# Kernel tuning notes

Measured on AMD Instinct MI355X. Metric: run time of the kernel, lower is better.

Reference implementation:

```python
import jax, jax.numpy as jnp
import numpy as np

THETA = 1.2
XI = 0.3


def setup_inputs() -> dict:
    key = jax.random.key(0)
    k1, k2 = jax.random.split(key)
    B, D = 8192, 512
    x = jax.random.normal(k1, (B, D), dtype=jnp.float32)
    y = jax.random.randint(k2, (B,), 0, 1000, dtype=jnp.int64)
    return {"x": x, "y": y}


def reference(x, y):
    B = x.shape[0]
    # per-sample L2 normalization: n_i = x_i / ||x_i||
    n = x / jnp.linalg.norm(x, axis=1, keepdims=True)  # [B, D]
    # pairwise squared distances ||n_i - n_j||^2 = |n_i|^2 + |n_j|^2 - 2 n_i.n_j
    sq = jnp.sum(n * n, axis=1)                        # [B]
    G = n @ n.T                                        # [B, B]
    dist2 = sq[:, None] + sq[None, :] - 2.0 * G        # [B, B]
    # indicator: +1 if same label else -1 (symmetric)
    ind = jnp.where(y[:, None] == y[None, :], 1.0, -1.0)
    # original loops i in [0,B), j in [i,B): upper triangle including diagonal
    idx = jnp.arange(B)
    mask = (idx[None, :] >= idx[:, None]).astype(x.dtype)
    hinge = jnp.maximum(THETA - dist2, 0.0)
    total = jnp.sum(mask * (XI + ind * hinge))
    m_scalar = 1.0 / (B * B - B)
    return m_scalar * total
```

## Files before the change

### kernel.cpp

```cpp
#include <hip/hip_runtime.h>
#include <cstdint>
#include <cstddef>

#define THETA 1.2f
#define XI 0.3f
#define BDIM 8192
#define DDIM 512
#define NROWP 32
#define NCOLP 64
#define NUNITS 1056
#define GRID 512
#define NPAIRS_UP (((double)BDIM * (double)(BDIM + 1)) * 0.5)

typedef float f32x4 __attribute__((ext_vector_type(4)));
typedef int i32x8 __attribute__((ext_vector_type(8)));


__global__ __launch_bounds__(256) void normalize_rows(
    const float* __restrict__ x, unsigned char* __restrict__ nf8,
    float* __restrict__ sq, unsigned int* __restrict__ counter)
{
    if (blockIdx.x == 0 && threadIdx.x == 0) { *counter = 0u; }
    int row = blockIdx.x * 4 + (threadIdx.x >> 6);
    int l = threadIdx.x & 63;
    const float4* xr = (const float4*)(x + (size_t)row * DDIM);
    float4 f0 = xr[l];
    float4 f1 = xr[l + 64];
    float s = f0.x*f0.x + f0.y*f0.y + f0.z*f0.z + f0.w*f0.w
            + f1.x*f1.x + f1.y*f1.y + f1.z*f1.z + f1.w*f1.w;
    #pragma unroll
    for (int m = 1; m < 64; m <<= 1) s += __shfl_xor(s, m);
    float rn = rsqrtf(s);
    int pk0 = __builtin_amdgcn_cvt_pk_fp8_f32(f0.x * rn, f0.y * rn, 0, false);
    pk0     = __builtin_amdgcn_cvt_pk_fp8_f32(f0.z * rn, f0.w * rn, pk0, true);
    int pk1 = __builtin_amdgcn_cvt_pk_fp8_f32(f1.x * rn, f1.y * rn, 0, false);
    pk1     = __builtin_amdgcn_cvt_pk_fp8_f32(f1.z * rn, f1.w * rn, pk1, true);
    size_t base = (size_t)(row >> 4) * 4 * 2048;
    int within = ((row & 15) + ((l >> 3) & 3) * 16) * 32 + (l & 7) * 4;
    int kc0 = l >> 5;
    int kc1 = (l >> 5) + 2;
    *(int*)(nf8 + base + (size_t)kc0 * 2048 + within) = pk0;
    *(int*)(nf8 + base + (size_t)kc1 * 2048 + within) = pk1;
    if (l == 0) sq[row] = s * rn * rn;
}

__device__ __forceinline__ void decode_unit(int u, int& ti, int& tj) {
    int t = (int)((65.0f - sqrtf(65.0f * 65.0f - 4.0f * (float)u)) * 0.5f);
    if (t > 31) t = 31;
    while (t < 31 && (t + 1) * (65 - (t + 1)) <= u) ++t;
    while (t > 0 && t * (65 - t) > u) --t;
    ti = t;
    tj = 2 * t + (u - t * (65 - t));
}

__global__ __launch_bounds__(512, 2) void gram_hinge(
    const unsigned char* __restrict__ nf8, const float* __restrict__ sq,
    const int* __restrict__ y, double* __restrict__ part,
    unsigned int* __restrict__ counter, float* __restrict__ out)
{
    __shared__ unsigned char As[2][32768];
    __shared__ float wpart[8];
    __shared__ double dpart[8];
    __shared__ int is_last;

    int tid = threadIdx.x;
    int w = tid >> 6, l = tid & 63;
    int wr = w >> 2, wc = w & 3;
    int lr = l & 15, q = l >> 4;

    auto stageA = [&](unsigned char* dAb, int pti, int pc) {
        #pragma unroll
        for (int i = 0; i < 4; ++i) {
            int t = w * 4 + i;
            int rf = t >> 1, half = t & 1;
            const unsigned char* src = nf8
                + ((size_t)((pti * 16 + rf) * 4 + pc)) * 2048 + half * 1024 + l * 16;
            __builtin_amdgcn_global_load_lds(
                (const __attribute__((address_space(1))) void*)src,
                (__attribute__((address_space(3))) void*)(dAb + t * 1024), 16, 0, 0);
        }
    };
    auto bload = [&](int ptj, int pc, i32x8* dst) {
        #pragma unroll
        for (int ni = 0; ni < 2; ++ni)
            dst[ni] = *(const i32x8*)(nf8
                + ((size_t)((ptj * 8 + wc * 2 + ni) * 4 + pc)) * 2048 + l * 32);
    };

    float acc0 = 0.f, acc1 = 0.f;

    int u = blockIdx.x;
    int ti, tj;
    decode_unit(u, ti, tj);

    i32x8 bfe[2], bfo[2];

    bload(tj, 0, bfe);
    stageA(As[0], ti, 0);

    while (u < NUNITS) {
        int u_next = u + GRID;
        bool have_next = (u_next < NUNITS);
        int ti_n = 0, tj_n = 0;
        if (have_next) decode_unit(u_next, ti_n, tj_n);

        f32x4 accv[8][2] = {};

        #pragma unroll 1
        for (int cc = 0; cc < 2; ++cc) {
            bload(tj, 2 * cc + 1, bfo);
            stageA(As[1], ti, 2 * cc + 1);
            asm volatile("s_waitcnt vmcnt(8)" ::: "memory");
            asm volatile("s_barrier" ::: "memory");
            __builtin_amdgcn_s_setprio(1);
            #pragma unroll
            for (int mi = 0; mi < 8; ++mi) {
                i32x8 af = *(const i32x8*)(As[0] + (wr * 8 + mi) * 2048 + l * 32);
                #pragma unroll
                for (int ni = 0; ni < 2; ++ni)
                    accv[mi][ni] = __builtin_amdgcn_mfma_scale_f32_16x16x128_f8f6f4(
                        af, bfe[ni], accv[mi][ni],
                        0, 0, 0, 0x7F7F7F7F, 0, 0x7F7F7F7F);
            }
            __builtin_amdgcn_s_setprio(0);
            asm volatile("s_barrier" ::: "memory");

            bool more = (cc == 0) || have_next;
            int nti = (cc == 0) ? ti : ti_n;
            int ntj = (cc == 0) ? tj : tj_n;
            int nc  = (cc == 0) ? 2 : 0;
            if (more) {
                bload(ntj, nc, bfe);
                stageA(As[0], nti, nc);
                asm volatile("s_waitcnt vmcnt(8)" ::: "memory");
            } else {
                asm volatile("s_waitcnt vmcnt(0)" ::: "memory");
            }
            asm volatile("s_barrier" ::: "memory");
            __builtin_amdgcn_s_setprio(1);
            #pragma unroll
            for (int mi = 0; mi < 8; ++mi) {
                i32x8 af = *(const i32x8*)(As[1] + (wr * 8 + mi) * 2048 + l * 32);
                #pragma unroll
                for (int ni = 0; ni < 2; ++ni)
                    accv[mi][ni] = __builtin_amdgcn_mfma_scale_f32_16x16x128_f8f6f4(
                        af, bfo[ni], accv[mi][ni],
                        0, 0, 0, 0x7F7F7F7F, 0, 0x7F7F7F7F);
            }
            __builtin_amdgcn_s_setprio(0);
            asm volatile("s_barrier" ::: "memory");
        }

        {
            int jb = tj * 128 + wc * 32 + lr;
            float sqj[2]; int yj[2];
            #pragma unroll
            for (int ni = 0; ni < 2; ++ni) {
                sqj[ni] = sq[jb + ni * 16];
                yj[ni]  = y[jb + ni * 16];
            }
            bool skip = (tj == 2 * ti) && (wr == 1);
            bool full = (tj > 2 * ti + 1) || ((tj == 2 * ti + 1) && (wr == 0));
            if (!skip) {
                if (full) {
                    #pragma unroll
                    for (int mi = 0; mi < 8; ++mi) {
                        #pragma unroll
                        for (int r = 0; r < 4; ++r) {
                            int ia = ti * 256 + wr * 128 + mi * 16 + q * 4 + r;
                            float ci = THETA - sq[ia];
                            int yi = y[ia];
                            float h0 = fmaxf(fmaf(2.f, accv[mi][0][r], ci - sqj[0]), 0.f);
                            acc0 += (yi == yj[0]) ? h0 : -h0;
                            float h1 = fmaxf(fmaf(2.f, accv[mi][1][r], ci - sqj[1]), 0.f);
                            acc1 += (yi == yj[1]) ? h1 : -h1;
                        }
                    }
                } else {
                    #pragma unroll
                    for (int mi = 0; mi < 8; ++mi) {
                        #pragma unroll
                        for (int r = 0; r < 4; ++r) {
                            int rl_ = mi * 16 + q * 4 + r;
                            int ia = ti * 256 + wr * 128 + rl_;
                            float ci = THETA - sq[ia];
                            int yi = y[ia];
                            #pragma unroll
                            for (int ni = 0; ni < 2; ++ni) {
                                float h = fmaxf(fmaf(2.f, accv[mi][ni][r], ci - sqj[ni]), 0.f);
                                float sh = (yi == yj[ni]) ? h : -h;
                                if (wc * 32 + ni * 16 + lr >= rl_) acc0 += sh;
                            }
                        }
                    }
                }
            }
        }

        u = u_next; ti = ti_n; tj = tj_n;
    }

    float local = acc0 + acc1;
    #pragma unroll
    for (int off = 32; off > 0; off >>= 1) local += __shfl_down(local, off);
    if (l == 0) wpart[w] = local;
    __syncthreads();
    if (tid == 0) {
        double ssum = 0.0;
        #pragma unroll
        for (int i = 0; i < 8; ++i) ssum += (double)wpart[i];
        __hip_atomic_store(&part[blockIdx.x], ssum, __ATOMIC_RELEASE, __HIP_MEMORY_SCOPE_AGENT);
        unsigned int ticket = __hip_atomic_fetch_add(
            counter, 1u, __ATOMIC_ACQ_REL, __HIP_MEMORY_SCOPE_AGENT);
        is_last = (ticket == GRID - 1) ? 1 : 0;
    }
    __syncthreads();
    if (is_last) {
        double s = 0.0;
        for (int i = tid; i < GRID; i += 512)
            s += __hip_atomic_load(&part[i], __ATOMIC_ACQUIRE, __HIP_MEMORY_SCOPE_AGENT);
        #pragma unroll
        for (int off = 32; off > 0; off >>= 1) s += __shfl_down(s, off);
        if (l == 0) dpart[w] = s;
        __syncthreads();
        if (tid == 0) {
            double t8 = 0.0;
            #pragma unroll
            for (int i = 0; i < 8; ++i) t8 += dpart[i];
            double total = t8 + (double)XI * NPAIRS_UP;
            const double m = 1.0 / ((double)BDIM * (double)BDIM - (double)BDIM);
            out[0] = (float)(total * m);
        }
    }
}

extern "C" void kernel_launch(void* const* d_in, const int* in_sizes, int n_in,
                              void* d_out, int out_size, void* d_ws, size_t ws_size,
                              hipStream_t stream) {
    const float* x = (const float*)d_in[0];
    const int* y = (const int*)d_in[1];
    float* out = (float*)d_out;

    unsigned char* nf8 = (unsigned char*)d_ws;
    char* p = (char*)d_ws + (size_t)BDIM * DDIM;
    float* sq = (float*)p;
    unsigned int* counter = (unsigned int*)(p + (size_t)BDIM * 4);
    double* part = (double*)(p + (size_t)BDIM * 4 + 64);

    normalize_rows<<<BDIM / 4, 256, 0, stream>>>(x, nf8, sq, counter);
    gram_hinge<<<GRID, 512, 0, stream>>>(nf8, sq, y, part, counter, out);
}
```

Before: 117.3 us.

## Use square 256x256 tiles with B staged in LDS instead of 256x128

Changes the work unit from 256x128 tiles to 256x256 tiles over the upper triangle, halving the number of units and the grid size. The B operand is now staged through LDS with async global-to-LDS loads alongside A, rather than each wave loading B fragments straight from global memory into registers. The intent is higher arithmetic intensity per byte loaded and less redundant global traffic for B. The cost is twice the LDS footprint, 32 accumulator vectors per wave with more register pressure, and a grid of only 256 blocks, which may underfill the device.

Result: faster. 107.0 us (-8.8%).

```diff
diff --git a/kernel.cpp b/kernel.cpp
--- a/kernel.cpp
+++ b/kernel.cpp
@@ -6,10 +6,9 @@
 #define XI 0.3f
 #define BDIM 8192
 #define DDIM 512
-#define NROWP 32
-#define NCOLP 64
-#define NUNITS 1056
-#define GRID 512
+#define NPANEL 32
+#define NUNITS 528
+#define GRID 256
 #define NPAIRS_UP (((double)BDIM * (double)(BDIM + 1)) * 0.5)
 
 typedef float f32x4 __attribute__((ext_vector_type(4)));
@@ -45,12 +44,13 @@
 }
 
 __device__ __forceinline__ void decode_unit(int u, int& ti, int& tj) {
-    int t = (int)((65.0f - sqrtf(65.0f * 65.0f - 4.0f * (float)u)) * 0.5f);
+    int t = (int)((65.0f - sqrtf(4225.0f - 8.0f * (float)u)) * 0.5f);
+    if (t < 0) t = 0;
     if (t > 31) t = 31;
-    while (t < 31 && (t + 1) * (65 - (t + 1)) <= u) ++t;
-    while (t > 0 && t * (65 - t) > u) --t;
+    while (t < 31 && (t + 1) * (65 - (t + 1)) / 2 <= u) ++t;
+    while (t > 0 && t * (65 - t) / 2 > u) --t;
     ti = t;
-    tj = 2 * t + (u - t * (65 - t));
+    tj = t + (u - t * (65 - t) / 2);
 }
 
 __global__ __launch_bounds__(512, 2) void gram_hinge(
@@ -59,6 +59,7 @@
     unsigned int* __restrict__ counter, float* __restrict__ out)
 {
     __shared__ unsigned char As[2][32768];
+    __shared__ unsigned char Bs[2][32768];
     __shared__ float wpart[8];
     __shared__ double dpart[8];
     __shared__ int is_last;
@@ -68,35 +69,32 @@
     int wr = w >> 2, wc = w & 3;
     int lr = l & 15, q = l >> 4;
 
-    auto stageA = [&](unsigned char* dAb, int pti, int pc) {
+    auto stage = [&](unsigned char* dA, unsigned char* dB,
+                     int pti, int ptj, int kc) {
         #pragma unroll
         for (int i = 0; i < 4; ++i) {
             int t = w * 4 + i;
             int rf = t >> 1, half = t & 1;
-            const unsigned char* src = nf8
-                + ((size_t)((pti * 16 + rf) * 4 + pc)) * 2048 + half * 1024 + l * 16;
+            const unsigned char* sA = nf8
+                + ((size_t)((pti * 16 + rf) * 4 + kc)) * 2048 + half * 1024 + l * 16;
+            const unsigned char* sB = nf8
+                + ((size_t)((ptj * 16 + rf) * 4 + kc)) * 2048 + half * 1024 + l * 16;
             __builtin_amdgcn_global_load_lds(
-                (const __attribute__((address_space(1))) void*)src,
-                (__attribute__((address_space(3))) void*)(dAb + t * 1024), 16, 0, 0);
+                (const __attribute__((address_space(1))) void*)sA,
+                (__attribute__((address_space(3))) void*)(dA + t * 1024), 16, 0, 0);
+            __builtin_amdgcn_global_load_lds(
+                (const __attribute__((address_space(1))) void*)sB,
+                (__attribute__((address_space(3))) void*)(dB + t * 1024), 16, 0, 0);
         }
     };
-    auto bload = [&](int ptj, int pc, i32x8* dst) {
-        #pragma unroll
-        for (int ni = 0; ni < 2; ++ni)
-            dst[ni] = *(const i32x8*)(nf8
-                + ((size_t)((ptj * 8 + wc * 2 + ni) * 4 + pc)) * 2048 + l * 32);
-    };
-
-    float acc0 = 0.f, acc1 = 0.f;
+
+    float acc0 = 0.f, acc1 = 0.f, acc2 = 0.f, acc3 = 0.f;
 
     int u = blockIdx.x;
     int ti, tj;
     decode_unit(u, ti, tj);
 
-    i32x8 bfe[2], bfo[2];
-
-    bload(tj, 0, bfe);
-    stageA(As[0], ti, 0);
+    stage(As[0], Bs[0], ti, tj, 0);
 
     while (u < NUNITS) {
         int u_next = u + GRID;
@@ -104,25 +102,30 @@
         int ti_n = 0, tj_n = 0;
         if (have_next) decode_unit(u_next, ti_n, tj_n);
 
-        f32x4 accv[8][2] = {};
+        f32x4 accv[8][4] = {};
 
         #pragma unroll 1
         for (int cc = 0; cc < 2; ++cc) {
-            bload(tj, 2 * cc + 1, bfo);
-            stageA(As[1], ti, 2 * cc + 1);
+            stage(As[1], Bs[1], ti, tj, 2 * cc + 1);
             asm volatile("s_waitcnt vmcnt(8)" ::: "memory");
             asm volatile("s_barrier" ::: "memory");
-            __builtin_amdgcn_s_setprio(1);
-            #pragma unroll
-            for (int mi = 0; mi < 8; ++mi) {
-                i32x8 af = *(const i32x8*)(As[0] + (wr * 8 + mi) * 2048 + l * 32);
-                #pragma unroll
-                for (int ni = 0; ni < 2; ++ni)
-                    accv[mi][ni] = __builtin_amdgcn_mfma_scale_f32_16x16x128_f8f6f4(
-                        af, bfe[ni], accv[mi][ni],
-                        0, 0, 0, 0x7F7F7F7F, 0, 0x7F7F7F7F);
-            }
-            __builtin_amdgcn_s_setprio(0);
+            {
+                i32x8 bf[4];
+                #pragma unroll
+                for (int ni = 0; ni < 4; ++ni)
+                    bf[ni] = *(const i32x8*)(Bs[0] + (wc * 4 + ni) * 2048 + l * 32);
+                __builtin_amdgcn_s_setprio(1);
+                #pragma unroll
+                for (int mi = 0; mi < 8; ++mi) {
+                    i32x8 af = *(const i32x8*)(As[0] + (wr * 8 + mi) * 2048 + l * 32);
+                    #pragma unroll
+                    for (int ni = 0; ni < 4; ++ni)
+                        accv[mi][ni] = __builtin_amdgcn_mfma_scale_f32_16x16x128_f8f6f4(
+                            af, bf[ni], accv[mi][ni],
+                            0, 0, 0, 0x7F7F7F7F, 0, 0x7F7F7F7F);
+                }
+                __builtin_amdgcn_s_setprio(0);
+            }
             asm volatile("s_barrier" ::: "memory");
 
             bool more = (cc == 0) || have_next;
@@ -130,37 +133,42 @@
             int ntj = (cc == 0) ? tj : tj_n;
             int nc  = (cc == 0) ? 2 : 0;
             if (more) {
-                bload(ntj, nc, bfe);
-                stageA(As[0], nti, nc);
+                stage(As[0], Bs[0], nti, ntj, nc);
                 asm volatile("s_waitcnt vmcnt(8)" ::: "memory");
             } else {
                 asm volatile("s_waitcnt vmcnt(0)" ::: "memory");
             }
             asm volatile("s_barrier" ::: "memory");
-            __builtin_amdgcn_s_setprio(1);
+            {
+                i32x8 bf[4];
+                #pragma unroll
+                for (int ni = 0; ni < 4; ++ni)
+                    bf[ni] = *(const i32x8*)(Bs[1] + (wc * 4 + ni) * 2048 + l * 32);
+                __builtin_amdgcn_s_setprio(1);
+                #pragma unroll
+                for (int mi = 0; mi < 8; ++mi) {
+                    i32x8 af = *(const i32x8*)(As[1] + (wr * 8 + mi) * 2048 + l * 32);
+                    #pragma unroll
+                    for (int ni = 0; ni < 4; ++ni)
+                        accv[mi][ni] = __builtin_amdgcn_mfma_scale_f32_16x16x128_f8f6f4(
+                            af, bf[ni], accv[mi][ni],
+                            0, 0, 0, 0x7F7F7F7F, 0, 0x7F7F7F7F);
+                }
+                __builtin_amdgcn_s_setprio(0);
+            }
+            asm volatile("s_barrier" ::: "memory");
+        }
+
+        {
+            int jb = tj * 256 + wc * 64 + lr;
+            float sqj[4]; int yj[4];
             #pragma unroll
-            for (int mi = 0; mi < 8; ++mi) {
-                i32x8 af = *(const i32x8*)(As[1] + (wr * 8 + mi) * 2048 + l * 32);
-                #pragma unroll
-                for (int ni = 0; ni < 2; ++ni)
-                    accv[mi][ni] = __builtin_amdgcn_mfma_scale_f32_16x16x128_f8f6f4(
-                        af, bfo[ni], accv[mi][ni],
-                        0, 0, 0, 0x7F7F7F7F, 0, 0x7F7F7F7F);
-            }
-            __builtin_amdgcn_s_setprio(0);
-            asm volatile("s_barrier" ::: "memory");
-        }
-
-        {
-            int jb = tj * 128 + wc * 32 + lr;
-            float sqj[2]; int yj[2];
-            #pragma unroll
-            for (int ni = 0; ni < 2; ++ni) {
+            for (int ni = 0; ni < 4; ++ni) {
                 sqj[ni] = sq[jb + ni * 16];
                 yj[ni]  = y[jb + ni * 16];
             }
-            bool skip = (tj == 2 * ti) && (wr == 1);
-            bool full = (tj > 2 * ti + 1) || ((tj == 2 * ti + 1) && (wr == 0));
+            bool skip = (ti == tj) && (wr == 1) && (wc < 2);
+            bool full = (ti != tj) || ((wr == 0) && (wc >= 2));
             if (!skip) {
                 if (full) {
                     #pragma unroll
@@ -174,6 +182,10 @@
                             acc0 += (yi == yj[0]) ? h0 : -h0;
                             float h1 = fmaxf(fmaf(2.f, accv[mi][1][r], ci - sqj[1]), 0.f);
                             acc1 += (yi == yj[1]) ? h1 : -h1;
+                            float h2 = fmaxf(fmaf(2.f, accv[mi][2][r], ci - sqj[2]), 0.f);
+                            acc2 += (yi == yj[2]) ? h2 : -h2;
+                            float h3 = fmaxf(fmaf(2.f, accv[mi][3][r], ci - sqj[3]), 0.f);
+                            acc3 += (yi == yj[3]) ? h3 : -h3;
                         }
                     }
                 } else {
@@ -181,15 +193,14 @@
                     for (int mi = 0; mi < 8; ++mi) {
                         #pragma unroll
                         for (int r = 0; r < 4; ++r) {
-                            int rl_ = mi * 16 + q * 4 + r;
-                            int ia = ti * 256 + wr * 128 + rl_;
+                            int ia = ti * 256 + wr * 128 + mi * 16 + q * 4 + r;
                             float ci = THETA - sq[ia];
                             int yi = y[ia];
                             #pragma unroll
-                            for (int ni = 0; ni < 2; ++ni) {
+                            for (int ni = 0; ni < 4; ++ni) {
                                 float h = fmaxf(fmaf(2.f, accv[mi][ni][r], ci - sqj[ni]), 0.f);
                                 float sh = (yi == yj[ni]) ? h : -h;
-                                if (wc * 32 + ni * 16 + lr >= rl_) acc0 += sh;
+                                if (jb + ni * 16 >= ia) acc0 += sh;
                             }
                         }
                     }
@@ -200,7 +211,7 @@
         u = u_next; ti = ti_n; tj = tj_n;
     }
 
-    float local = acc0 + acc1;
+    float local = (acc0 + acc1) + (acc2 + acc3);
     #pragma unroll
     for (int off = 32; off > 0; off >>= 1) local += __shfl_down(local, off);
     if (l == 0) wpart[w] = local;
```
